# Kernel tuning notes

Measured on AMD Instinct MI355X. Metric: run time of the kernel, lower is better.

The kernel has to match this reference:

```python
import jax, jax.numpy as jnp
import numpy as np

M_MARGIN = 0.2   # Config.MARGIN_ARCFACE
S_SCALE = 16.0   # Config.SCALE_ARCFACE
EPS = 1e-7
L2_EPS = 1e-12   # torch F.normalize eps

N, D, C = 8192, 512, 32000


def _l2_normalize(x, axis=-1):
    # matches torch F.normalize: x / max(||x||, eps)
    norm = jnp.sqrt(jnp.sum(x * x, axis=axis, keepdims=True))
    return x / jnp.maximum(norm, L2_EPS)


def setup_inputs() -> dict:
    key = jax.random.key(0)
    k1, k2, k3 = jax.random.split(key, 3)
    prev_output = jax.random.normal(k1, (N, D), dtype=jnp.float32)
    # xavier_uniform_ init for weight [C, D]
    limit = float(np.sqrt(6.0 / (C + D)))
    weight = jax.random.uniform(k2, (C, D), dtype=jnp.float32, minval=-limit, maxval=limit)
    labels = jax.random.randint(k3, (N,), 0, C, dtype=jnp.int64)
    return {"prev_output": prev_output, "weight": weight, "labels": labels}


def reference(prev_output, weight, labels):
    x = _l2_normalize(prev_output)          # [N, D]
    w = _l2_normalize(weight)               # [C, D]
    cosine = jnp.einsum('nd,cd->nc', x, w)  # [N, C]
    theta = jnp.arccos(jnp.clip(cosine, -1.0 + EPS, 1.0 - EPS))
    margin_logits = jnp.cos(theta + M_MARGIN)
    one_hot = (jnp.arange(cosine.shape[1])[None, :] == labels[:, None])
    logits = jnp.where(one_hot, margin_logits, cosine) * S_SCALE
    logp = jax.nn.log_softmax(logits, axis=-1)
    nll = -jnp.take_along_axis(logp, labels[:, None], axis=1)[:, 0]
    return jnp.mean(nll)
```

## Files before the change

### kernel.cpp

```cpp
#include <hip/hip_runtime.h>


typedef __attribute__((ext_vector_type(4))) float f32x4;
typedef __attribute__((ext_vector_type(16))) float f32x16;
typedef __attribute__((ext_vector_type(4))) int i32x4;
typedef __attribute__((ext_vector_type(8))) int i32x8;

constexpr int N = 8192, D = 512, C = 32000;
constexpr int BM = 128;
constexpr int NSPLIT = 16;
constexpr int CPS = C / NSPLIT;
constexpr int GCH = 63;
constexpr int KS8 = 8;
constexpr float SCL = 16.0f;
constexpr float LOG2E = 1.4426950408889634f;
constexpr float S2 = SCL * LOG2E;
constexpr float COSM = 0.98006657784124163f;
constexpr float SINM = 0.19866933079506122f;
constexpr float EPSC = 1e-7f;
constexpr float EM16 = 1.12535174719259114e-07f;
constexpr float FEC = 1064871712.0f;

__device__ __forceinline__ unsigned enc_fp4(float v, float inv) {
  unsigned s = (__float_as_uint(v) >> 31) << 3;
  float m = fabsf(v) * inv;
  float r = m < 2.0f ? 2.0f * m : (m < 4.0f ? m + 2.0f : fmaf(m, 0.5f, 4.0f));
  unsigned q = (unsigned)(r + 0.5f);
  return s | (q > 7u ? 7u : q);
}

__device__ __forceinline__ void block_scale(float amax, unsigned& eB, float& inv) {
  unsigned u = __float_as_uint(amax * (1.0f / 6.0f));
  eB = (u >> 23) & 255u;
  if (u & 0x7fffffu) eB += 1u;
  if (eB < 1u) eB = 1u;
  if (eB > 254u) eB = 254u;
  inv = __uint_as_float((254u - eB) << 23);
}

__device__ __forceinline__ i32x8 up8(i32x4 v) {
  return __builtin_shufflevector(v, v, 0, 1, 2, 3, -1, -1, -1, -1);
}

__global__ void k_norm_x(const float* __restrict__ in, unsigned* __restrict__ xn4,
                         unsigned char* __restrict__ xsc, float* __restrict__ outz) {
  if (blockIdx.x == 0 && threadIdx.x == 0) *outz = 0.0f;
  int w = (blockIdx.x << 2) + (threadIdx.x >> 6);
  int L = threadIdx.x & 63;
  const float* row = in + (size_t)w * D;
  float f[8];
  *(f32x4*)&f[0] = *(const f32x4*)(row + L * 8);
  *(f32x4*)&f[4] = *(const f32x4*)(row + L * 8 + 4);
  float ss = 0.f;
  #pragma unroll
  for (int i = 0; i < 8; ++i) ss += f[i] * f[i];
  #pragma unroll
  for (int m = 1; m <= 32; m <<= 1) ss += __shfl_xor(ss, m, 64);
  float sc = S2 / fmaxf(sqrtf(ss), 1e-12f);
  float v[8], am = 0.f;
  #pragma unroll
  for (int i = 0; i < 8; ++i) { v[i] = f[i] * sc; am = fmaxf(am, fabsf(v[i])); }
  am = fmaxf(am, __shfl_xor(am, 1, 64));
  am = fmaxf(am, __shfl_xor(am, 2, 64));
  unsigned eB; float inv;
  block_scale(am, eB, inv);
  unsigned pk = 0;
  #pragma unroll
  for (int j = 0; j < 8; ++j) pk |= enc_fp4(v[j], inv) << (4 * j);
  xn4[(size_t)w * 64 + L] = pk;
  if ((L & 3) == 0) {
    int kb = L >> 2;
    xsc[(size_t)w * 16 + (kb & 1) * 8 + (kb >> 1)] = (unsigned char)eB;
  }
}

__global__ void k_normw_t(const float* __restrict__ in, unsigned char* __restrict__ wt4,
                          unsigned char* __restrict__ wsc) {
  __shared__ unsigned lbuf[2048];
  __shared__ unsigned char sbuf[512];
  const int tid = threadIdx.x, wv = tid >> 6, L = tid & 63;
  const int gidx = blockIdx.x;
  const int sp = gidx / GCH, within = gidx % GCH;
  #pragma unroll
  for (int t = 0; t < 8; ++t) {
    int rl = t * 4 + wv;
    int colin = within * 32 + rl;
    bool valid = colin < CPS;
    unsigned pk = 0;
    unsigned eB = 1u;
    if (valid) {
      const float* row = in + ((size_t)sp * CPS + colin) * D;
      float f[8];
      *(f32x4*)&f[0] = *(const f32x4*)(row + L * 8);
      *(f32x4*)&f[4] = *(const f32x4*)(row + L * 8 + 4);
      float ss = 0.f;
      #pragma unroll
      for (int i = 0; i < 8; ++i) ss += f[i] * f[i];
      #pragma unroll
      for (int m = 1; m <= 32; m <<= 1) ss += __shfl_xor(ss, m, 64);
      float sc = 1.0f / fmaxf(sqrtf(ss), 1e-12f);
      float v[8], am = 0.f;
      #pragma unroll
      for (int i = 0; i < 8; ++i) { v[i] = f[i] * sc; am = fmaxf(am, fabsf(v[i])); }
      am = fmaxf(am, __shfl_xor(am, 1, 64));
      am = fmaxf(am, __shfl_xor(am, 2, 64));
      float inv;
      block_scale(am, eB, inv);
      #pragma unroll
      for (int j = 0; j < 8; ++j) pk |= enc_fp4(v[j], inv) << (4 * j);
    }
    lbuf[(L >> 3) * 256 + (((L >> 2) & 1) * 32 + rl) * 4 + (L & 3)] = pk;
    if ((L & 3) == 0) {
      int kb = L >> 2;
      sbuf[rl * 16 + (kb & 1) * 8 + (kb >> 1)] = (unsigned char)eB;
    }
  }
  __syncthreads();
  uint4* dst = (uint4*)(wt4 + (size_t)gidx * 8192);
  #pragma unroll
  for (int i = 0; i < 2; ++i) dst[i * 256 + tid] = ((const uint4*)lbuf)[i * 256 + tid];
  if (tid < 128)
    ((unsigned*)(wsc + (size_t)gidx * 512))[tid] = ((const unsigned*)sbuf)[tid];
}

__global__ void k_lab(const float* __restrict__ x, const float* __restrict__ w,
                      const int* __restrict__ labels, float* __restrict__ coslab) {
  int r = (blockIdx.x << 2) + (threadIdx.x >> 6);
  int lane = threadIdx.x & 63;
  const float* xr = x + (size_t)r * D;
  const float* wr = w + (size_t)labels[r] * D;
  f32x4 a = *(const f32x4*)(xr + lane * 8);
  f32x4 b = *(const f32x4*)(xr + lane * 8 + 4);
  f32x4 p = *(const f32x4*)(wr + lane * 8);
  f32x4 q = *(const f32x4*)(wr + lane * 8 + 4);
  float xx = a.x*a.x + a.y*a.y + a.z*a.z + a.w*a.w + b.x*b.x + b.y*b.y + b.z*b.z + b.w*b.w;
  float ww = p.x*p.x + p.y*p.y + p.z*p.z + p.w*p.w + q.x*q.x + q.y*q.y + q.z*q.z + q.w*q.w;
  float xw = a.x*p.x + a.y*p.y + a.z*p.z + a.w*p.w + b.x*q.x + b.y*q.y + b.z*q.z + b.w*q.w;
  #pragma unroll
  for (int m = 1; m <= 32; m <<= 1) {
    xx += __shfl_xor(xx, m, 64);
    ww += __shfl_xor(ww, m, 64);
    xw += __shfl_xor(xw, m, 64);
  }
  if (lane == 0)
    coslab[r] = xw / (fmaxf(sqrtf(xx), 1e-12f) * fmaxf(sqrtf(ww), 1e-12f));
}

#define KS_STEP(KSL, CHNEXT)                                                  \
    __builtin_amdgcn_s_setprio(1);                                            \
    acc = __builtin_amdgcn_mfma_scale_f32_32x32x64_f8f6f4(                    \
        up8(af4[KSL]), up8(b4[KSL]), (KSL) == 0 ? fzero : acc,                \
        4, 4, (KSL) & 3, ((KSL) >> 2) ? ascB : ascA,                          \
              (KSL) & 3, ((KSL) >> 2) ? bscB : bscA);                         \
    __builtin_amdgcn_s_setprio(0);                                            \
    b4[KSL] = *(const i32x4*)(gb + (size_t)(CHNEXT) * 8192 + (KSL) * 1024);

#define CHUNK_STEP(CHNEXT)                                                    \
  {                                                                           \
    int nscA = *(const int*)(gsc + (size_t)(CHNEXT) * 512);                   \
    int nscB = *(const int*)(gsc + (size_t)(CHNEXT) * 512 + 4);               \
    KS_STEP(0, CHNEXT)                                                        \
    KS_STEP(1, CHNEXT)                                                        \
    KS_STEP(2, CHNEXT)                                                        \
    KS_STEP(3, CHNEXT)                                                        \
    KS_STEP(4, CHNEXT)                                                        \
    KS_STEP(5, CHNEXT)                                                        \
    KS_STEP(6, CHNEXT)                                                        \
    KS_STEP(7, CHNEXT)                                                        \
    _Pragma("unroll")                                                         \
    for (int i = 0; i < 16; ++i)                                              \
      accS[i] += __uint_as_float((unsigned)fmaf(acc[i], 8388608.0f, FEC));    \
    bscA = nscA; bscB = nscB;                                                 \
  }

__global__ __launch_bounds__(256, 4) void k_fused(
    const unsigned char* __restrict__ xn4, const unsigned char* __restrict__ xsc,
    const unsigned char* __restrict__ wt4, const unsigned char* __restrict__ wsc,
    float* __restrict__ pS) {
  const int tid = threadIdx.x;
  const int wv = tid >> 6, lane = tid & 63;
  const int h = lane >> 5, c = lane & 31;
  const int bid = blockIdx.x;
  const int logical = (bid & 7) * 128 + (bid >> 3);
  const int sp = logical >> 6;
  const int rb = logical & 63;
  const int row0 = rb * BM + wv * 32;

  i32x4 af4[KS8];
  int ascA, ascB;
  {
    const unsigned char* xr = xn4 + (size_t)(row0 + c) * 256 + h * 16;
    #pragma unroll
    for (int ks = 0; ks < KS8; ++ks) af4[ks] = *(const i32x4*)(xr + ks * 32);
    ascA = *(const int*)(xsc + (size_t)(row0 + c) * 16 + h * 8);
    ascB = *(const int*)(xsc + (size_t)(row0 + c) * 16 + h * 8 + 4);
  }

  float accS[16];
  #pragma unroll
  for (int i = 0; i < 16; ++i) accS[i] = 0.0f;

  const f32x16 fzero = (f32x16)0.0f;

  const unsigned char* gb = wt4 + (size_t)(sp * GCH) * 8192 + lane * 16;
  const unsigned char* gsc = wsc + (size_t)(sp * GCH) * 512 + c * 16 + h * 8;

  i32x4 b4[KS8];
  #pragma unroll
  for (int ks = 0; ks < KS8; ++ks) b4[ks] = *(const i32x4*)(gb + ks * 1024);
  int bscA = *(const int*)gsc;
  int bscB = *(const int*)(gsc + 4);

  f32x16 acc;

  for (int ch = 0; ch < GCH; ++ch) {
    int cn = ch + 1 < GCH ? ch + 1 : GCH - 1;
    CHUNK_STEP(cn)
  }

  #pragma unroll
  for (int i = 0; i < 16; ++i) {
    float S = accS[i];
    #pragma unroll
    for (int m = 1; m <= 16; m <<= 1) S += __shfl_xor(S, m, 64);
    accS[i] = S;
  }
  if (c == 0) {
    #pragma unroll
    for (int i = 0; i < 16; ++i) {
      int rl = (i & 3) + 8 * (i >> 2) + 4 * h;
      pS[(size_t)sp * N + row0 + rl] = accS[i];
    }
  }
}
#undef CHUNK_STEP
#undef KS_STEP

__global__ void k_merge(const float* __restrict__ pS, const float* __restrict__ coslab,
                        float* __restrict__ out) {
  int row = blockIdx.x * 256 + threadIdx.x;
  float S = 0.0f;
  #pragma unroll
  for (int s = 0; s < NSPLIT; ++s) S += pS[(size_t)s * N + row];
  S -= 256.0f * __uint_as_float((unsigned)FEC);
  float cl = coslab[row];
  float zp = SCL * cl;
  float ccl = fminf(fmaxf(cl, -1.0f + EPSC), 1.0f - EPSC);
  float zm = SCL * (ccl * COSM - sqrtf(1.0f - ccl * ccl) * SINM);
  float denom = S * EM16 - __expf(zp - SCL) + __expf(zm - SCL);
  float nll = SCL + logf(denom) - zm;
  #pragma unroll
  for (int m = 1; m <= 32; m <<= 1) nll += __shfl_xor(nll, m, 64);
  __shared__ float part[4];
  if ((threadIdx.x & 63) == 0) part[threadIdx.x >> 6] = nll;
  __syncthreads();
  if (threadIdx.x == 0)
    atomicAdd(out, (part[0] + part[1] + part[2] + part[3]) * (1.0f / N));
}

extern "C" void kernel_launch(void* const* d_in, const int* in_sizes, int n_in,
                              void* d_out, int out_size, void* d_ws, size_t ws_size,
                              hipStream_t stream) {
  const float* x = (const float*)d_in[0];
  const float* w = (const float*)d_in[1];
  const int* labels = (const int*)d_in[2];
  float* out = (float*)d_out;

  unsigned char* xn4 = (unsigned char*)d_ws;
  unsigned char* xsc = xn4 + (size_t)N * 256;
  unsigned char* wt4 = xsc + (size_t)N * 16;
  unsigned char* wsc = wt4 + (size_t)NSPLIT * GCH * 8192;
  float* pS = (float*)(wsc + (size_t)NSPLIT * GCH * 512);
  float* coslab = pS + (size_t)NSPLIT * N;

  hipLaunchKernelGGL(k_norm_x, dim3(N / 4), dim3(256), 0, stream,
                     x, (unsigned*)xn4, xsc, out);
  hipLaunchKernelGGL(k_normw_t, dim3(NSPLIT * GCH), dim3(256), 0, stream, w, wt4, wsc);
  hipLaunchKernelGGL(k_lab, dim3(N / 4), dim3(256), 0, stream, x, w, labels, coslab);
  hipLaunchKernelGGL(k_fused, dim3(64 * NSPLIT), dim3(256), 0, stream,
                     xn4, xsc, wt4, wsc, pS);
  hipLaunchKernelGGL(k_merge, dim3(N / 256), dim3(256), 0, stream, pS, coslab, out);
}
```

Before: 117.5 us.

## Compute two 32-row tiles per wave to reuse each streamed weight fragment

Each wave now holds A fragments for 64 rows instead of 32 and issues two scaled MFMAs per loaded B fragment, so every weight chunk fetched from global memory feeds twice the work. The block tile grows to 256 rows and the grid halves to 512 blocks, with launch bounds lowered to 2 blocks per SM to leave room for the extra registers. This aims to cut weight-streaming traffic and load latency per MFMA, at the cost of fewer resident waves and a grid that may underfill the 256 CUs.

```diff
diff --git a/kernel.cpp b/kernel.cpp
--- a/kernel.cpp
+++ b/kernel.cpp
@@ -7,7 +7,7 @@
 typedef __attribute__((ext_vector_type(8))) int i32x8;
 
 constexpr int N = 8192, D = 512, C = 32000;
-constexpr int BM = 128;
+constexpr int BM = 256;
 constexpr int NSPLIT = 16;
 constexpr int CPS = C / NSPLIT;
 constexpr int GCH = 63;
@@ -148,9 +148,13 @@
 
 #define KS_STEP(KSL, CHNEXT)                                                  \
     __builtin_amdgcn_s_setprio(1);                                            \
-    acc = __builtin_amdgcn_mfma_scale_f32_32x32x64_f8f6f4(                    \
-        up8(af4[KSL]), up8(b4[KSL]), (KSL) == 0 ? fzero : acc,                \
-        4, 4, (KSL) & 3, ((KSL) >> 2) ? ascB : ascA,                          \
+    acc0 = __builtin_amdgcn_mfma_scale_f32_32x32x64_f8f6f4(                   \
+        up8(af4[0][KSL]), up8(b4[KSL]), (KSL) == 0 ? fzero : acc0,            \
+        4, 4, (KSL) & 3, ((KSL) >> 2) ? ascB0 : ascA0,                        \
+              (KSL) & 3, ((KSL) >> 2) ? bscB : bscA);                         \
+    acc1 = __builtin_amdgcn_mfma_scale_f32_32x32x64_f8f6f4(                   \
+        up8(af4[1][KSL]), up8(b4[KSL]), (KSL) == 0 ? fzero : acc1,            \
+        4, 4, (KSL) & 3, ((KSL) >> 2) ? ascB1 : ascA1,                        \
               (KSL) & 3, ((KSL) >> 2) ? bscB : bscA);                         \
     __builtin_amdgcn_s_setprio(0);                                            \
     b4[KSL] = *(const i32x4*)(gb + (size_t)(CHNEXT) * 8192 + (KSL) * 1024);
@@ -168,12 +172,14 @@
     KS_STEP(6, CHNEXT)                                                        \
     KS_STEP(7, CHNEXT)                                                        \
     _Pragma("unroll")                                                         \
-    for (int i = 0; i < 16; ++i)                                              \
-      accS[i] += __uint_as_float((unsigned)fmaf(acc[i], 8388608.0f, FEC));    \
+    for (int i = 0; i < 16; ++i) {                                            \
+      accS0[i] += __uint_as_float((unsigned)fmaf(acc0[i], 8388608.0f, FEC));  \
+      accS1[i] += __uint_as_float((unsigned)fmaf(acc1[i], 8388608.0f, FEC));  \
+    }                                                                         \
     bscA = nscA; bscB = nscB;                                                 \
   }
 
-__global__ __launch_bounds__(256, 4) void k_fused(
+__global__ __launch_bounds__(256, 2) void k_fused(
     const unsigned char* __restrict__ xn4, const unsigned char* __restrict__ xsc,
     const unsigned char* __restrict__ wt4, const unsigned char* __restrict__ wsc,
     float* __restrict__ pS) {
@@ -181,24 +187,30 @@
   const int wv = tid >> 6, lane = tid & 63;
   const int h = lane >> 5, c = lane & 31;
   const int bid = blockIdx.x;
-  const int logical = (bid & 7) * 128 + (bid >> 3);
-  const int sp = logical >> 6;
-  const int rb = logical & 63;
-  const int row0 = rb * BM + wv * 32;
-
-  i32x4 af4[KS8];
-  int ascA, ascB;
+  const int logical = (bid & 7) * 64 + (bid >> 3);
+  const int sp = logical >> 5;
+  const int rb = logical & 31;
+  const int row0 = rb * BM + wv * 64;
+
+  i32x4 af4[2][KS8];
+  int ascA0, ascB0, ascA1, ascB1;
   {
-    const unsigned char* xr = xn4 + (size_t)(row0 + c) * 256 + h * 16;
+    const unsigned char* x0 = xn4 + (size_t)(row0 + c) * 256 + h * 16;
+    const unsigned char* x1 = xn4 + (size_t)(row0 + 32 + c) * 256 + h * 16;
     #pragma unroll
-    for (int ks = 0; ks < KS8; ++ks) af4[ks] = *(const i32x4*)(xr + ks * 32);
-    ascA = *(const int*)(xsc + (size_t)(row0 + c) * 16 + h * 8);
-    ascB = *(const int*)(xsc + (size_t)(row0 + c) * 16 + h * 8 + 4);
-  }
-
-  float accS[16];
-  #pragma unroll
-  for (int i = 0; i < 16; ++i) accS[i] = 0.0f;
+    for (int ks = 0; ks < KS8; ++ks) {
+      af4[0][ks] = *(const i32x4*)(x0 + ks * 32);
+      af4[1][ks] = *(const i32x4*)(x1 + ks * 32);
+    }
+    ascA0 = *(const int*)(xsc + (size_t)(row0 + c) * 16 + h * 8);
+    ascB0 = *(const int*)(xsc + (size_t)(row0 + c) * 16 + h * 8 + 4);
+    ascA1 = *(const int*)(xsc + (size_t)(row0 + 32 + c) * 16 + h * 8);
+    ascB1 = *(const int*)(xsc + (size_t)(row0 + 32 + c) * 16 + h * 8 + 4);
+  }
+
+  float accS0[16], accS1[16];
+  #pragma unroll
+  for (int i = 0; i < 16; ++i) { accS0[i] = 0.0f; accS1[i] = 0.0f; }
 
   const f32x16 fzero = (f32x16)0.0f;
 
@@ -211,7 +223,7 @@
   int bscA = *(const int*)gsc;
   int bscB = *(const int*)(gsc + 4);
 
-  f32x16 acc;
+  f32x16 acc0, acc1;
 
   for (int ch = 0; ch < GCH; ++ch) {
     int cn = ch + 1 < GCH ? ch + 1 : GCH - 1;
@@ -220,16 +232,20 @@
 
   #pragma unroll
   for (int i = 0; i < 16; ++i) {
-    float S = accS[i];
+    float S0 = accS0[i], S1 = accS1[i];
     #pragma unroll
-    for (int m = 1; m <= 16; m <<= 1) S += __shfl_xor(S, m, 64);
-    accS[i] = S;
+    for (int m = 1; m <= 16; m <<= 1) {
+      S0 += __shfl_xor(S0, m, 64);
+      S1 += __shfl_xor(S1, m, 64);
+    }
+    accS0[i] = S0; accS1[i] = S1;
   }
   if (c == 0) {
     #pragma unroll
     for (int i = 0; i < 16; ++i) {
       int rl = (i & 3) + 8 * (i >> 2) + 4 * h;
-      pS[(size_t)sp * N + row0 + rl] = accS[i];
+      pS[(size_t)sp * N + row0 + rl] = accS0[i];
+      pS[(size_t)sp * N + row0 + 32 + rl] = accS1[i];
     }
   }
 }
@@ -277,7 +293,7 @@
                      x, (unsigned*)xn4, xsc, out);
   hipLaunchKernelGGL(k_normw_t, dim3(NSPLIT * GCH), dim3(256), 0, stream, w, wt4, wsc);
   hipLaunchKernelGGL(k_lab, dim3(N / 4), dim3(256), 0, stream, x, w, labels, coslab);
-  hipLaunchKernelGGL(k_fused, dim3(64 * NSPLIT), dim3(256), 0, stream,
+  hipLaunchKernelGGL(k_fused, dim3(32 * NSPLIT), dim3(256), 0, stream,
                      xn4, xsc, wt4, wsc, pS);
   hipLaunchKernelGGL(k_merge, dim3(N / 256), dim3(256), 0, stream, pS, coslab, out);
 }
```

Result: faster. 103.8 us (-11.7%).
